# Kernel tuning notes

Measured on AMD Instinct MI355X. Metric: run time of the kernel, lower is better.

## Reference

```python
import jax, jax.numpy as jnp
import numpy as np

BN_EPS = 1e-5


def setup_inputs() -> dict:
    key = jax.random.key(0)
    ks = jax.random.split(key, 8)
    N, C, H, W = 16, 64, 56, 56
    Ch = C // 2
    x = jax.random.normal(ks[0], (N, C, H, W), dtype=jnp.float32)
    # 1x1 convs represented as [out, in] matrices
    w1 = jax.random.normal(ks[1], (Ch, C), dtype=jnp.float32) / np.sqrt(C)
    b1 = jnp.zeros((Ch,), dtype=jnp.float32)
    w2 = jax.random.normal(ks[2], (Ch, C), dtype=jnp.float32) / np.sqrt(C)
    b2 = jnp.zeros((Ch,), dtype=jnp.float32)
    w3 = jax.random.normal(ks[3], (C, C), dtype=jnp.float32) / np.sqrt(C)
    b3 = jnp.zeros((C,), dtype=jnp.float32)
    gamma = jnp.ones((C,), dtype=jnp.float32)
    beta = jnp.zeros((C,), dtype=jnp.float32)
    return {"x": x, "w1": w1, "b1": b1, "w2": w2, "b2": b2,
            "w3": w3, "b3": b3, "gamma": gamma, "beta": beta}


def _conv1x1(x, w, b):
    # x: [N,C,H,W], w: [O,C] -> [N,O,H,W]
    return jnp.einsum('nchw,oc->nohw', x, w) + b[None, :, None, None]


def reference(x, w1, b1, w2, b2, w3, b3, gamma, beta):
    N, C, H, W = x.shape
    S = H * W
    theta = _conv1x1(x, w1, b1)            # [N, C/2, H, W]
    phi = _conv1x1(x, w2, b2)              # [N, C/2, H, W]
    g = x                                  # [N, C, H, W]
    th = theta.reshape(N, -1, S)           # [N, C/2, S]
    ph = phi.reshape(N, -1, S)             # [N, C/2, S]
    gf = g.reshape(N, C, S)                # [N, C, S]
    scale = 1.0 / jnp.sqrt(jnp.float32(th.shape[1]))
    attn = jnp.einsum('nis,nit->nst', th, ph) * scale   # [N, S, S]
    attn = jax.nn.softmax(attn, axis=-1)
    f = jnp.einsum('nst,nit->nis', attn, gf).reshape(N, C, H, W)
    f = _conv1x1(f, w3, b3)
    # BatchNorm2d, training mode (batch statistics, biased variance)
    mean = jnp.mean(f, axis=(0, 2, 3), keepdims=True)
    var = jnp.mean((f - mean) ** 2, axis=(0, 2, 3), keepdims=True)
    f = (f - mean) / jnp.sqrt(var + BN_EPS)
    f = f * gamma[None, :, None, None] + beta[None, :, None, None]
    return x + f
```

## Files before the change

kernel.cpp:

```cpp
#include <hip/hip_runtime.h>
#include <hip/hip_bf16.h>

constexpr int N_ = 16, C_ = 64, CH_ = 32;
constexpr int S_ = 3136;
constexpr int SB = 64;
constexpr int NB = S_ / SB;
constexpr float SCALE = 0.17677669529663687f;
constexpr float LOG2E = 1.4426950408889634f;
constexpr float SCALE2 = SCALE * LOG2E;
constexpr float FIXM2 = 16.0f * LOG2E;

using f32x4 = __attribute__((ext_vector_type(4))) float;
using bf16x8 = __attribute__((ext_vector_type(8))) short;
using u32x2 = __attribute__((ext_vector_type(2))) unsigned;
using u32x4 = __attribute__((ext_vector_type(4))) unsigned;

__device__ __forceinline__ unsigned cvtpk(float lo, float hi) {
  unsigned r;
  asm("v_cvt_pk_bf16_f32 %0, %1, %2" : "=v"(r) : "v"(lo), "v"(hi));
  return r;
}
__device__ __forceinline__ float exp2a(float x) {
  float r;
  asm("v_exp_f32 %0, %1" : "=v"(r) : "v"(x));
  return r;
}
__device__ __forceinline__ unsigned short f2bf(float f) {
  unsigned int u = __builtin_bit_cast(unsigned int, f);
  u += 0x7fffu + ((u >> 16) & 1u);
  return (unsigned short)(u >> 16);
}

__global__ __launch_bounds__(256)
void prep_kernel(const float* __restrict__ x,
                 const float* __restrict__ w1, const float* __restrict__ b1,
                 const float* __restrict__ w2, const float* __restrict__ b2,
                 unsigned short* __restrict__ thetaT,
                 unsigned short* __restrict__ phiT,
                 unsigned short* __restrict__ xbf) {
  __shared__ float xl[64][68];
  __shared__ __align__(16) unsigned short thL[64][40];
  __shared__ __align__(16) unsigned short phL[64][40];
  const int b = blockIdx.x;
  const int n = b / NB;
  const int s0 = (b % NB) * SB;
  const int tid = threadIdx.x;
  const int sl = tid & 63;
  const int grp = tid >> 6;

#pragma unroll
  for (int cc = 0; cc < 4; ++cc) {
    int c = cc * 16 + grp * 4 + (sl >> 4);
    int s4 = (sl & 15) * 4;
    size_t gidx = (size_t)(n * C_ + c) * S_ + s0 + s4;
    f32x4 v = *(const f32x4*)(x + gidx);
    *(f32x4*)&xl[c][s4] = v;
    u32x2 pb;
    pb.x = cvtpk(v[0], v[1]);
    pb.y = cvtpk(v[2], v[3]);
    *(u32x2*)(xbf + gidx) = pb;
  }
  __syncthreads();

  float acc1[8], acc2[8];
  const int i0u = __builtin_amdgcn_readfirstlane(grp * 8);
  const float* w1b = w1 + i0u * C_;
  const float* w2b = w2 + i0u * C_;
#pragma unroll
  for (int ii = 0; ii < 8; ++ii) {
    acc1[ii] = b1[i0u + ii];
    acc2[ii] = b2[i0u + ii];
  }
#pragma unroll 1
  for (int cc = 0; cc < 4; ++cc) {
    float xv[16];
#pragma unroll
    for (int k = 0; k < 16; ++k) xv[k] = xl[cc * 16 + k][sl];
#pragma unroll
    for (int ii = 0; ii < 8; ++ii) {
#pragma unroll
      for (int k = 0; k < 16; ++k) {
        acc1[ii] = fmaf(w1b[ii * C_ + cc * 16 + k], xv[k], acc1[ii]);
        acc2[ii] = fmaf(w2b[ii * C_ + cc * 16 + k], xv[k], acc2[ii]);
      }
    }
  }
  {
    u32x4 t4, p4;
    t4.x = cvtpk(acc1[0] * SCALE2, acc1[1] * SCALE2);
    t4.y = cvtpk(acc1[2] * SCALE2, acc1[3] * SCALE2);
    t4.z = cvtpk(acc1[4] * SCALE2, acc1[5] * SCALE2);
    t4.w = cvtpk(acc1[6] * SCALE2, acc1[7] * SCALE2);
    p4.x = cvtpk(acc2[0], acc2[1]);
    p4.y = cvtpk(acc2[2], acc2[3]);
    p4.z = cvtpk(acc2[4], acc2[5]);
    p4.w = cvtpk(acc2[6], acc2[7]);
    *(u32x4*)&thL[sl][grp * 8] = t4;
    *(u32x4*)&phL[sl][grp * 8] = p4;
  }
  __syncthreads();
  {
    int row = tid >> 2, ch = (tid & 3) * 8;
    size_t o = ((size_t)(n * S_) + s0 + row) * CH_ + ch;
    *(bf16x8*)(thetaT + o) = *(const bf16x8*)&thL[row][ch];
    *(bf16x8*)(phiT + o)   = *(const bf16x8*)&phL[row][ch];
  }
}

__global__ __launch_bounds__(256)
void attn_kernel(const unsigned short* __restrict__ thetaT,
                 const unsigned short* __restrict__ phiT,
                 const unsigned short* __restrict__ xbf,
                 const float* __restrict__ w3, const float* __restrict__ b3,
                 unsigned short* __restrict__ yb, float* __restrict__ partials) {
  __shared__ __align__(16) unsigned short ldsK[2][64 * 40];
  __shared__ __align__(16) unsigned short ldsV[2][64 * 72];
  __shared__ float redS[4][128];
  const int b = (blockIdx.x & 7) * 98 + (blockIdx.x >> 3);
  const int n = b / NB;
  const int q0 = (b % NB) * SB;
  const int tid = threadIdx.x;
  const int lane = tid & 63;
  const int w = tid >> 6;
  const int l16 = lane & 15;
  const int g = lane >> 4;

  const bf16x8 qf = *(const bf16x8*)(thetaT + ((size_t)(n * S_) + q0 + w * 16 + l16) * CH_ + g * 8);

  f32x4 oacc[4];
#pragma unroll
  for (int r = 0; r < 4; ++r) oacc[r] = (f32x4){0.f, 0.f, 0.f, 0.f};
  float lsum = 0.f;
  const f32x4 cinit = (f32x4){-FIXM2, -FIXM2, -FIXM2, -FIXM2};

  const unsigned short* phiB = phiT + (size_t)n * S_ * CH_;
  const unsigned short* vB = xbf + (size_t)n * C_ * S_;

  const int krow = tid >> 2, kch = (tid & 3) * 8;
  const int vc = tid >> 3, vch = (tid & 7) * 8;

  bf16x8 kst, vst0, vst1;
  kst = *(const bf16x8*)(phiB + (size_t)krow * CH_ + kch);
  vst0 = *(const bf16x8*)(vB + (size_t)vc * S_ + vch);
  vst1 = *(const bf16x8*)(vB + (size_t)(vc + 32) * S_ + vch);
  *(bf16x8*)(ldsK[0] + krow * 40 + kch) = kst;
  *(bf16x8*)(ldsV[0] + vc * 72 + vch) = vst0;
  *(bf16x8*)(ldsV[0] + (vc + 32) * 72 + vch) = vst1;
  __syncthreads();

  int cur = 0;
#pragma unroll 1
  for (int t0 = 0; t0 < S_; t0 += 64) {
    const bool pre = (t0 + 64 < S_);
    if (pre) {
      kst = *(const bf16x8*)(phiB + (size_t)(t0 + 64 + krow) * CH_ + kch);
      vst0 = *(const bf16x8*)(vB + (size_t)vc * S_ + t0 + 64 + vch);
      vst1 = *(const bf16x8*)(vB + (size_t)(vc + 32) * S_ + t0 + 64 + vch);
    }

    const unsigned short* Kc = ldsK[cur];
    const unsigned short* Vc = ldsV[cur];
    f32x4 st[4];
    __builtin_amdgcn_s_setprio(1);
#pragma unroll
    for (int tt = 0; tt < 4; ++tt) {
      bf16x8 kf = *(const bf16x8*)(Kc + (tt * 16 + l16) * 40 + g * 8);
      st[tt] = __builtin_amdgcn_mfma_f32_16x16x32_bf16(kf, qf, cinit, 0, 0, 0);
    }
    __builtin_amdgcn_s_setprio(0);

    u32x2 pk[4];
#pragma unroll
    for (int tt = 0; tt < 4; ++tt) {
      float p0 = exp2a(st[tt][0]);
      float p1 = exp2a(st[tt][1]);
      float p2 = exp2a(st[tt][2]);
      float p3 = exp2a(st[tt][3]);
      lsum += (p0 + p1) + (p2 + p3);
      pk[tt].x = cvtpk(p0, p1);
      pk[tt].y = cvtpk(p2, p3);
    }

    __builtin_amdgcn_s_setprio(1);
#pragma unroll
    for (int h = 0; h < 2; ++h) {
      bf16x8 pf = __builtin_bit_cast(bf16x8,
          (u32x4){pk[2 * h].x, pk[2 * h].y, pk[2 * h + 1].x, pk[2 * h + 1].y});
#pragma unroll
      for (int ct = 0; ct < 4; ++ct) {
        const unsigned short* vrow = Vc + (ct * 16 + l16) * 72 + 32 * h + 4 * g;
        u32x2 v0 = *(const u32x2*)(vrow);
        u32x2 v1 = *(const u32x2*)(vrow + 16);
        bf16x8 vf = __builtin_bit_cast(bf16x8, (u32x4){v0.x, v0.y, v1.x, v1.y});
        oacc[ct] = __builtin_amdgcn_mfma_f32_16x16x32_bf16(vf, pf, oacc[ct], 0, 0, 0);
      }
    }
    __builtin_amdgcn_s_setprio(0);

    if (pre) {
      *(bf16x8*)(ldsK[cur ^ 1] + krow * 40 + kch) = kst;
      *(bf16x8*)(ldsV[cur ^ 1] + vc * 72 + vch) = vst0;
      *(bf16x8*)(ldsV[cur ^ 1] + (vc + 32) * 72 + vch) = vst1;
    }
    __syncthreads();
    cur ^= 1;
  }

  float lt = lsum;
  lt += __shfl_xor(lt, 16);
  lt += __shfl_xor(lt, 32);
  const float inv = 1.0f / lt;

  u32x4 ff[2];
#pragma unroll
  for (int m = 0; m < 2; ++m) {
    ff[m].x = cvtpk(oacc[2 * m][0] * inv, oacc[2 * m][1] * inv);
    ff[m].y = cvtpk(oacc[2 * m][2] * inv, oacc[2 * m][3] * inv);
    ff[m].z = cvtpk(oacc[2 * m + 1][0] * inv, oacc[2 * m + 1][1] * inv);
    ff[m].w = cvtpk(oacc[2 * m + 1][2] * inv, oacc[2 * m + 1][3] * inv);
  }

  const int q = q0 + w * 16 + l16;
#pragma unroll
  for (int t = 0; t < 4; ++t) {
    const float* wr = w3 + (t * 16 + l16) * C_;
    f32x4 acc = *(const f32x4*)(b3 + t * 16 + 4 * g);
#pragma unroll
    for (int m = 0; m < 2; ++m) {
      f32x4 A0 = *(const f32x4*)(wr + 32 * m + 4 * g);
      f32x4 A1 = *(const f32x4*)(wr + 32 * m + 16 + 4 * g);
      u32x4 wf;
      wf.x = cvtpk(A0[0], A0[1]);
      wf.y = cvtpk(A0[2], A0[3]);
      wf.z = cvtpk(A1[0], A1[1]);
      wf.w = cvtpk(A1[2], A1[3]);
      acc = __builtin_amdgcn_mfma_f32_16x16x32_bf16(
          __builtin_bit_cast(bf16x8, wf), __builtin_bit_cast(bf16x8, ff[m]),
          acc, 0, 0, 0);
    }
#pragma unroll
    for (int rd = 0; rd < 4; ++rd) {
      const int co = t * 16 + 4 * g + rd;
      float yv = acc[rd];
      yb[(size_t)(n * C_ + co) * S_ + q] = f2bf(yv);
      float s1 = yv, s2 = yv * yv;
#pragma unroll
      for (int off = 1; off < 16; off <<= 1) {
        s1 += __shfl_xor(s1, off);
        s2 += __shfl_xor(s2, off);
      }
      if (l16 == 0) {
        redS[w][co] = s1;
        redS[w][64 + co] = s2;
      }
    }
  }
  __syncthreads();
  if (tid < 128)
    partials[(size_t)b * 128 + tid] =
        redS[0][tid] + redS[1][tid] + redS[2][tid] + redS[3][tid];
}

__global__ __launch_bounds__(256)
void stats_kernel(const float* __restrict__ partials, float* __restrict__ stats) {
  __shared__ float red[4];
  const int c = blockIdx.x;
  const int tid = threadIdx.x;
  float s = 0.f;
  for (int r = tid; r < N_ * NB; r += 256) s += partials[(size_t)r * 128 + c];
#pragma unroll
  for (int off = 1; off < 64; off <<= 1) s += __shfl_xor(s, off);
  if ((tid & 63) == 0) red[tid >> 6] = s;
  __syncthreads();
  if (tid == 0) stats[c] = red[0] + red[1] + red[2] + red[3];
}

__global__ __launch_bounds__(256)
void bn_kernel(const float* __restrict__ x, const unsigned short* __restrict__ yb,
               const float* __restrict__ stats,
               const float* __restrict__ gamma, const float* __restrict__ beta,
               float* __restrict__ out) {
  const int idx = blockIdx.x * 256 + threadIdx.x;
  const size_t base = (size_t)idx * 8;
  const int c = (int)((base / S_) & 63);
  constexpr float invcnt = 1.0f / (N_ * S_);
  float mean = stats[c] * invcnt;
  float var = stats[64 + c] * invcnt - mean * mean;
  float a = gamma[c] * rsqrtf(var + 1e-5f);
  float bb = beta[c] - mean * a;
  u32x4 yv = *(const u32x4*)(yb + base);
#pragma unroll
  for (int h = 0; h < 2; ++h) {
    f32x4 xv = *(const f32x4*)(x + base + h * 4);
    f32x4 o;
#pragma unroll
    for (int r = 0; r < 2; ++r) {
      unsigned packed = (h * 2 + r == 0) ? yv.x : (h * 2 + r == 1) ? yv.y
                        : (h * 2 + r == 2) ? yv.z : yv.w;
      float ylo = __builtin_bit_cast(float, packed << 16);
      float yhi = __builtin_bit_cast(float, packed & 0xffff0000u);
      o[r * 2 + 0] = fmaf(ylo, a, xv[r * 2 + 0] + bb);
      o[r * 2 + 1] = fmaf(yhi, a, xv[r * 2 + 1] + bb);
    }
    *(f32x4*)(out + base + h * 4) = o;
  }
}

extern "C" void kernel_launch(void* const* d_in, const int* in_sizes, int n_in,
                              void* d_out, int out_size, void* d_ws, size_t ws_size,
                              hipStream_t stream) {
  const float* x = (const float*)d_in[0];
  const float* w1 = (const float*)d_in[1];
  const float* b1 = (const float*)d_in[2];
  const float* w2 = (const float*)d_in[3];
  const float* b2 = (const float*)d_in[4];
  const float* w3 = (const float*)d_in[5];
  const float* b3 = (const float*)d_in[6];
  const float* gamma = (const float*)d_in[7];
  const float* beta = (const float*)d_in[8];

  char* ws = (char*)d_ws;
  unsigned short* thetaT = (unsigned short*)(ws + 0);
  unsigned short* phiT   = (unsigned short*)(ws + 3211264);
  unsigned short* xbf    = (unsigned short*)(ws + 6422528);
  unsigned short* yb     = (unsigned short*)(ws + 12845056);
  float* stats           = (float*)(ws + 19267584);
  float* partials        = (float*)(ws + 19268096);
  if (ws_size < 19669504) return;

  prep_kernel<<<N_ * NB, 256, 0, stream>>>(x, w1, b1, w2, b2, thetaT, phiT, xbf);
  attn_kernel<<<N_ * NB, 256, 0, stream>>>(thetaT, phiT, xbf, w3, b3, yb, partials);
  stats_kernel<<<128, 256, 0, stream>>>(partials, stats);
  bn_kernel<<<(out_size / 8) / 256, 256, 0, stream>>>(x, yb, stats, gamma, beta, (float*)d_out);
}
```

Before: 115.0 us.

## Split key loop across two wave groups in attention kernel and merge partials

```diff
diff --git a/kernel.cpp b/kernel.cpp
--- a/kernel.cpp
+++ b/kernel.cpp
@@ -107,7 +107,7 @@
   }
 }
 
-__global__ __launch_bounds__(256)
+__global__ __launch_bounds__(512)
 void attn_kernel(const unsigned short* __restrict__ thetaT,
                  const unsigned short* __restrict__ phiT,
                  const unsigned short* __restrict__ xbf,
@@ -122,10 +122,12 @@
   const int tid = threadIdx.x;
   const int lane = tid & 63;
   const int w = tid >> 6;
+  const int qw = w & 3;
+  const int th = w >> 2;
   const int l16 = lane & 15;
   const int g = lane >> 4;
 
-  const bf16x8 qf = *(const bf16x8*)(thetaT + ((size_t)(n * S_) + q0 + w * 16 + l16) * CH_ + g * 8);
+  const bf16x8 qf = *(const bf16x8*)(thetaT + ((size_t)(n * S_) + q0 + qw * 16 + l16) * CH_ + g * 8);
 
   f32x4 oacc[4];
 #pragma unroll
@@ -136,122 +138,145 @@
   const unsigned short* phiB = phiT + (size_t)n * S_ * CH_;
   const unsigned short* vB = xbf + (size_t)n * C_ * S_;
 
-  const int krow = tid >> 2, kch = (tid & 3) * 8;
-  const int vc = tid >> 3, vch = (tid & 7) * 8;
+  const int sh = tid >> 8;
+  const int st = tid & 255;
+  const int krow = st >> 2, kch = (st & 3) * 8;
+  const int vc = st >> 3, vch = (st & 7) * 8;
 
   bf16x8 kst, vst0, vst1;
-  kst = *(const bf16x8*)(phiB + (size_t)krow * CH_ + kch);
-  vst0 = *(const bf16x8*)(vB + (size_t)vc * S_ + vch);
-  vst1 = *(const bf16x8*)(vB + (size_t)(vc + 32) * S_ + vch);
-  *(bf16x8*)(ldsK[0] + krow * 40 + kch) = kst;
-  *(bf16x8*)(ldsV[0] + vc * 72 + vch) = vst0;
-  *(bf16x8*)(ldsV[0] + (vc + 32) * 72 + vch) = vst1;
-  __syncthreads();
-
-  int cur = 0;
+  {
+    const int t0s = sh * 64;
+    kst = *(const bf16x8*)(phiB + (size_t)(t0s + krow) * CH_ + kch);
+    vst0 = *(const bf16x8*)(vB + (size_t)vc * S_ + t0s + vch);
+    vst1 = *(const bf16x8*)(vB + (size_t)(vc + 32) * S_ + t0s + vch);
+    *(bf16x8*)(ldsK[sh] + krow * 40 + kch) = kst;
+    *(bf16x8*)(ldsV[sh] + vc * 72 + vch) = vst0;
+    *(bf16x8*)(ldsV[sh] + (vc + 32) * 72 + vch) = vst1;
+  }
+  __syncthreads();
+
 #pragma unroll 1
-  for (int t0 = 0; t0 < S_; t0 += 64) {
-    const bool pre = (t0 + 64 < S_);
+  for (int pb = 0; pb < S_; pb += 128) {
+    const int tpre = pb + 128 + sh * 64;
+    const bool pre = tpre < S_;
     if (pre) {
-      kst = *(const bf16x8*)(phiB + (size_t)(t0 + 64 + krow) * CH_ + kch);
-      vst0 = *(const bf16x8*)(vB + (size_t)vc * S_ + t0 + 64 + vch);
-      vst1 = *(const bf16x8*)(vB + (size_t)(vc + 32) * S_ + t0 + 64 + vch);
-    }
-
-    const unsigned short* Kc = ldsK[cur];
-    const unsigned short* Vc = ldsV[cur];
-    f32x4 st[4];
-    __builtin_amdgcn_s_setprio(1);
-#pragma unroll
-    for (int tt = 0; tt < 4; ++tt) {
-      bf16x8 kf = *(const bf16x8*)(Kc + (tt * 16 + l16) * 40 + g * 8);
-      st[tt] = __builtin_amdgcn_mfma_f32_16x16x32_bf16(kf, qf, cinit, 0, 0, 0);
-    }
-    __builtin_amdgcn_s_setprio(0);
-
-    u32x2 pk[4];
-#pragma unroll
-    for (int tt = 0; tt < 4; ++tt) {
-      float p0 = exp2a(st[tt][0]);
-      float p1 = exp2a(st[tt][1]);
-      float p2 = exp2a(st[tt][2]);
-      float p3 = exp2a(st[tt][3]);
-      lsum += (p0 + p1) + (p2 + p3);
-      pk[tt].x = cvtpk(p0, p1);
-      pk[tt].y = cvtpk(p2, p3);
-    }
-
-    __builtin_amdgcn_s_setprio(1);
-#pragma unroll
-    for (int h = 0; h < 2; ++h) {
-      bf16x8 pf = __builtin_bit_cast(bf16x8,
-          (u32x4){pk[2 * h].x, pk[2 * h].y, pk[2 * h + 1].x, pk[2 * h + 1].y});
-#pragma unroll
-      for (int ct = 0; ct < 4; ++ct) {
-        const unsigned short* vrow = Vc + (ct * 16 + l16) * 72 + 32 * h + 4 * g;
-        u32x2 v0 = *(const u32x2*)(vrow);
-        u32x2 v1 = *(const u32x2*)(vrow + 16);
-        bf16x8 vf = __builtin_bit_cast(bf16x8, (u32x4){v0.x, v0.y, v1.x, v1.y});
-        oacc[ct] = __builtin_amdgcn_mfma_f32_16x16x32_bf16(vf, pf, oacc[ct], 0, 0, 0);
-      }
-    }
-    __builtin_amdgcn_s_setprio(0);
-
+      kst = *(const bf16x8*)(phiB + (size_t)(tpre + krow) * CH_ + kch);
+      vst0 = *(const bf16x8*)(vB + (size_t)vc * S_ + tpre + vch);
+      vst1 = *(const bf16x8*)(vB + (size_t)(vc + 32) * S_ + tpre + vch);
+    }
+
+    const int t0 = pb + th * 64;
+    if (t0 < S_) {
+      const unsigned short* Kc = ldsK[th];
+      const unsigned short* Vc = ldsV[th];
+      f32x4 st4[4];
+      __builtin_amdgcn_s_setprio(1);
+#pragma unroll
+      for (int tt = 0; tt < 4; ++tt) {
+        bf16x8 kf = *(const bf16x8*)(Kc + (tt * 16 + l16) * 40 + g * 8);
+        st4[tt] = __builtin_amdgcn_mfma_f32_16x16x32_bf16(kf, qf, cinit, 0, 0, 0);
+      }
+      __builtin_amdgcn_s_setprio(0);
+
+      u32x2 pk[4];
+#pragma unroll
+      for (int tt = 0; tt < 4; ++tt) {
+        float p0 = exp2a(st4[tt][0]);
+        float p1 = exp2a(st4[tt][1]);
+        float p2 = exp2a(st4[tt][2]);
+        float p3 = exp2a(st4[tt][3]);
+        lsum += (p0 + p1) + (p2 + p3);
+        pk[tt].x = cvtpk(p0, p1);
+        pk[tt].y = cvtpk(p2, p3);
+      }
+
+      __builtin_amdgcn_s_setprio(1);
+#pragma unroll
+      for (int h = 0; h < 2; ++h) {
+        bf16x8 pf = __builtin_bit_cast(bf16x8,
+            (u32x4){pk[2 * h].x, pk[2 * h].y, pk[2 * h + 1].x, pk[2 * h + 1].y});
+#pragma unroll
+        for (int ct = 0; ct < 4; ++ct) {
+          const unsigned short* vrow = Vc + (ct * 16 + l16) * 72 + 32 * h + 4 * g;
+          u32x2 v0 = *(const u32x2*)(vrow);
+          u32x2 v1 = *(const u32x2*)(vrow + 16);
+          bf16x8 vf = __builtin_bit_cast(bf16x8, (u32x4){v0.x, v0.y, v1.x, v1.y});
+          oacc[ct] = __builtin_amdgcn_mfma_f32_16x16x32_bf16(vf, pf, oacc[ct], 0, 0, 0);
+        }
+      }
+      __builtin_amdgcn_s_setprio(0);
+    }
+
+    __syncthreads();
     if (pre) {
-      *(bf16x8*)(ldsK[cur ^ 1] + krow * 40 + kch) = kst;
-      *(bf16x8*)(ldsV[cur ^ 1] + vc * 72 + vch) = vst0;
-      *(bf16x8*)(ldsV[cur ^ 1] + (vc + 32) * 72 + vch) = vst1;
+      *(bf16x8*)(ldsK[sh] + krow * 40 + kch) = kst;
+      *(bf16x8*)(ldsV[sh] + vc * 72 + vch) = vst0;
+      *(bf16x8*)(ldsV[sh] + (vc + 32) * 72 + vch) = vst1;
     }
     __syncthreads();
-    cur ^= 1;
-  }
-
-  float lt = lsum;
-  lt += __shfl_xor(lt, 16);
-  lt += __shfl_xor(lt, 32);
-  const float inv = 1.0f / lt;
-
-  u32x4 ff[2];
-#pragma unroll
-  for (int m = 0; m < 2; ++m) {
-    ff[m].x = cvtpk(oacc[2 * m][0] * inv, oacc[2 * m][1] * inv);
-    ff[m].y = cvtpk(oacc[2 * m][2] * inv, oacc[2 * m][3] * inv);
-    ff[m].z = cvtpk(oacc[2 * m + 1][0] * inv, oacc[2 * m + 1][1] * inv);
-    ff[m].w = cvtpk(oacc[2 * m + 1][2] * inv, oacc[2 * m + 1][3] * inv);
-  }
-
-  const int q = q0 + w * 16 + l16;
-#pragma unroll
-  for (int t = 0; t < 4; ++t) {
-    const float* wr = w3 + (t * 16 + l16) * C_;
-    f32x4 acc = *(const f32x4*)(b3 + t * 16 + 4 * g);
+  }
+
+  float* mrg = (float*)&ldsV[0][0];
+  if (th == 1) {
+    float* p = mrg + ((size_t)(qw * 64 + lane)) * 18;
+#pragma unroll
+    for (int ct = 0; ct < 4; ++ct) *(f32x4*)(p + ct * 4) = oacc[ct];
+    p[16] = lsum;
+  }
+  __syncthreads();
+  if (th == 0) {
+    float* p = mrg + ((size_t)(qw * 64 + lane)) * 18;
+#pragma unroll
+    for (int ct = 0; ct < 4; ++ct) oacc[ct] += *(const f32x4*)(p + ct * 4);
+    lsum += p[16];
+
+    float lt = lsum;
+    lt += __shfl_xor(lt, 16);
+    lt += __shfl_xor(lt, 32);
+    const float inv = 1.0f / lt;
+
+    u32x4 ff[2];
 #pragma unroll
     for (int m = 0; m < 2; ++m) {
-      f32x4 A0 = *(const f32x4*)(wr + 32 * m + 4 * g);
-      f32x4 A1 = *(const f32x4*)(wr + 32 * m + 16 + 4 * g);
-      u32x4 wf;
-      wf.x = cvtpk(A0[0], A0[1]);
-      wf.y = cvtpk(A0[2], A0[3]);
-      wf.z = cvtpk(A1[0], A1[1]);
-      wf.w = cvtpk(A1[2], A1[3]);
-      acc = __builtin_amdgcn_mfma_f32_16x16x32_bf16(
-          __builtin_bit_cast(bf16x8, wf), __builtin_bit_cast(bf16x8, ff[m]),
-          acc, 0, 0, 0);
-    }
-#pragma unroll
-    for (int rd = 0; rd < 4; ++rd) {
-      const int co = t * 16 + 4 * g + rd;
-      float yv = acc[rd];
-      yb[(size_t)(n * C_ + co) * S_ + q] = f2bf(yv);
-      float s1 = yv, s2 = yv * yv;
-#pragma unroll
-      for (int off = 1; off < 16; off <<= 1) {
-        s1 += __shfl_xor(s1, off);
-        s2 += __shfl_xor(s2, off);
-      }
-      if (l16 == 0) {
-        redS[w][co] = s1;
-        redS[w][64 + co] = s2;
+      ff[m].x = cvtpk(oacc[2 * m][0] * inv, oacc[2 * m][1] * inv);
+      ff[m].y = cvtpk(oacc[2 * m][2] * inv, oacc[2 * m][3] * inv);
+      ff[m].z = cvtpk(oacc[2 * m + 1][0] * inv, oacc[2 * m + 1][1] * inv);
+      ff[m].w = cvtpk(oacc[2 * m + 1][2] * inv, oacc[2 * m + 1][3] * inv);
+    }
+
+    const int q = q0 + qw * 16 + l16;
+#pragma unroll
+    for (int t = 0; t < 4; ++t) {
+      const float* wr = w3 + (t * 16 + l16) * C_;
+      f32x4 acc = *(const f32x4*)(b3 + t * 16 + 4 * g);
+#pragma unroll
+      for (int m = 0; m < 2; ++m) {
+        f32x4 A0 = *(const f32x4*)(wr + 32 * m + 4 * g);
+        f32x4 A1 = *(const f32x4*)(wr + 32 * m + 16 + 4 * g);
+        u32x4 wf;
+        wf.x = cvtpk(A0[0], A0[1]);
+        wf.y = cvtpk(A0[2], A0[3]);
+        wf.z = cvtpk(A1[0], A1[1]);
+        wf.w = cvtpk(A1[2], A1[3]);
+        acc = __builtin_amdgcn_mfma_f32_16x16x32_bf16(
+            __builtin_bit_cast(bf16x8, wf), __builtin_bit_cast(bf16x8, ff[m]),
+            acc, 0, 0, 0);
+      }
+#pragma unroll
+      for (int rd = 0; rd < 4; ++rd) {
+        const int co = t * 16 + 4 * g + rd;
+        float yv = acc[rd];
+        yb[(size_t)(n * C_ + co) * S_ + q] = f2bf(yv);
+        float s1 = yv, s2 = yv * yv;
+#pragma unroll
+        for (int off = 1; off < 16; off <<= 1) {
+          s1 += __shfl_xor(s1, off);
+          s2 += __shfl_xor(s2, off);
+        }
+        if (l16 == 0) {
+          redS[qw][co] = s1;
+          redS[qw][64 + co] = s2;
+        }
       }
     }
   }
@@ -329,7 +354,7 @@
   if (ws_size < 19669504) return;
 
   prep_kernel<<<N_ * NB, 256, 0, stream>>>(x, w1, b1, w2, b2, thetaT, phiT, xbf);
-  attn_kernel<<<N_ * NB, 256, 0, stream>>>(thetaT, phiT, xbf, w3, b3, yb, partials);
+  attn_kernel<<<N_ * NB, 512, 0, stream>>>(thetaT, phiT, xbf, w3, b3, yb, partials);
   stats_kernel<<<128, 256, 0, stream>>>(partials, stats);
   bn_kernel<<<(out_size / 8) / 256, 256, 0, stream>>>(x, yb, stats, gamma, beta, (float*)d_out);
 }
```

Result: slower. 125.3 us (+8.9%).

## Switch attention to 32x32x16 MFMA with key-split waves and LDS merge

Applied to the files above, without the earlier changes.

```diff
diff --git a/kernel.cpp b/kernel.cpp
--- a/kernel.cpp
+++ b/kernel.cpp
@@ -11,6 +11,7 @@
 constexpr float FIXM2 = 16.0f * LOG2E;
 
 using f32x4 = __attribute__((ext_vector_type(4))) float;
+using f32x16 = __attribute__((ext_vector_type(16))) float;
 using bf16x8 = __attribute__((ext_vector_type(8))) short;
 using u32x2 = __attribute__((ext_vector_type(2))) unsigned;
 using u32x4 = __attribute__((ext_vector_type(4))) unsigned;
@@ -115,23 +116,32 @@
                  unsigned short* __restrict__ yb, float* __restrict__ partials) {
   __shared__ __align__(16) unsigned short ldsK[2][64 * 40];
   __shared__ __align__(16) unsigned short ldsV[2][64 * 72];
-  __shared__ float redS[4][128];
+  __shared__ float redS[2][128];
   const int b = (blockIdx.x & 7) * 98 + (blockIdx.x >> 3);
   const int n = b / NB;
   const int q0 = (b % NB) * SB;
   const int tid = threadIdx.x;
   const int lane = tid & 63;
   const int w = tid >> 6;
-  const int l16 = lane & 15;
-  const int g = lane >> 4;
-
-  const bf16x8 qf = *(const bf16x8*)(thetaT + ((size_t)(n * S_) + q0 + w * 16 + l16) * CH_ + g * 8);
-
-  f32x4 oacc[4];
-#pragma unroll
-  for (int r = 0; r < 4; ++r) oacc[r] = (f32x4){0.f, 0.f, 0.f, 0.f};
+  const int qw = w & 1;
+  const int th = w >> 1;
+  const int cl = lane & 31;
+  const int h = lane >> 5;
+
+  const unsigned short* thQ =
+      thetaT + ((size_t)(n * S_) + q0 + qw * 32 + cl) * CH_;
+  const bf16x8 qfA = *(const bf16x8*)(thQ + h * 8);
+  const bf16x8 qfB = *(const bf16x8*)(thQ + 16 + h * 8);
+
+  f32x16 oacc[2];
+#pragma unroll
+  for (int cb = 0; cb < 2; ++cb)
+#pragma unroll
+    for (int r = 0; r < 16; ++r) oacc[cb][r] = 0.f;
   float lsum = 0.f;
-  const f32x4 cinit = (f32x4){-FIXM2, -FIXM2, -FIXM2, -FIXM2};
+  f32x16 cinit;
+#pragma unroll
+  for (int r = 0; r < 16; ++r) cinit[r] = -FIXM2;
 
   const unsigned short* phiB = phiT + (size_t)n * S_ * CH_;
   const unsigned short* vB = xbf + (size_t)n * C_ * S_;
@@ -160,39 +170,38 @@
 
     const unsigned short* Kc = ldsK[cur];
     const unsigned short* Vc = ldsV[cur];
-    f32x4 st[4];
+
+    const unsigned short* kr = Kc + (th * 32 + cl) * 40 + h * 8;
+    bf16x8 kfA = *(const bf16x8*)(kr);
+    bf16x8 kfB = *(const bf16x8*)(kr + 16);
     __builtin_amdgcn_s_setprio(1);
-#pragma unroll
-    for (int tt = 0; tt < 4; ++tt) {
-      bf16x8 kf = *(const bf16x8*)(Kc + (tt * 16 + l16) * 40 + g * 8);
-      st[tt] = __builtin_amdgcn_mfma_f32_16x16x32_bf16(kf, qf, cinit, 0, 0, 0);
-    }
+    f32x16 st = __builtin_amdgcn_mfma_f32_32x32x16_bf16(kfA, qfA, cinit, 0, 0, 0);
+    st = __builtin_amdgcn_mfma_f32_32x32x16_bf16(kfB, qfB, st, 0, 0, 0);
     __builtin_amdgcn_s_setprio(0);
 
-    u32x2 pk[4];
-#pragma unroll
-    for (int tt = 0; tt < 4; ++tt) {
-      float p0 = exp2a(st[tt][0]);
-      float p1 = exp2a(st[tt][1]);
-      float p2 = exp2a(st[tt][2]);
-      float p3 = exp2a(st[tt][3]);
-      lsum += (p0 + p1) + (p2 + p3);
-      pk[tt].x = cvtpk(p0, p1);
-      pk[tt].y = cvtpk(p2, p3);
-    }
+    float p[16];
+#pragma unroll
+    for (int r = 0; r < 16; ++r) {
+      p[r] = exp2a(st[r]);
+      lsum += p[r];
+    }
+    unsigned pkw[8];
+#pragma unroll
+    for (int i = 0; i < 8; ++i) pkw[i] = cvtpk(p[2 * i], p[2 * i + 1]);
 
     __builtin_amdgcn_s_setprio(1);
 #pragma unroll
-    for (int h = 0; h < 2; ++h) {
+    for (int tb = 0; tb < 2; ++tb) {
       bf16x8 pf = __builtin_bit_cast(bf16x8,
-          (u32x4){pk[2 * h].x, pk[2 * h].y, pk[2 * h + 1].x, pk[2 * h + 1].y});
-#pragma unroll
-      for (int ct = 0; ct < 4; ++ct) {
-        const unsigned short* vrow = Vc + (ct * 16 + l16) * 72 + 32 * h + 4 * g;
-        u32x2 v0 = *(const u32x2*)(vrow);
-        u32x2 v1 = *(const u32x2*)(vrow + 16);
+          (u32x4){pkw[tb * 4 + 0], pkw[tb * 4 + 1], pkw[tb * 4 + 2], pkw[tb * 4 + 3]});
+#pragma unroll
+      for (int cb = 0; cb < 2; ++cb) {
+        const unsigned short* vr =
+            Vc + (cb * 32 + cl) * 72 + th * 32 + tb * 16 + 4 * h;
+        u32x2 v0 = *(const u32x2*)(vr);
+        u32x2 v1 = *(const u32x2*)(vr + 8);
         bf16x8 vf = __builtin_bit_cast(bf16x8, (u32x4){v0.x, v0.y, v1.x, v1.y});
-        oacc[ct] = __builtin_amdgcn_mfma_f32_16x16x32_bf16(vf, pf, oacc[ct], 0, 0, 0);
+        oacc[cb] = __builtin_amdgcn_mfma_f32_32x32x16_bf16(vf, pf, oacc[cb], 0, 0, 0);
       }
     }
     __builtin_amdgcn_s_setprio(0);
@@ -206,59 +215,101 @@
     cur ^= 1;
   }
 
-  float lt = lsum;
-  lt += __shfl_xor(lt, 16);
-  lt += __shfl_xor(lt, 32);
-  const float inv = 1.0f / lt;
-
-  u32x4 ff[2];
-#pragma unroll
-  for (int m = 0; m < 2; ++m) {
-    ff[m].x = cvtpk(oacc[2 * m][0] * inv, oacc[2 * m][1] * inv);
-    ff[m].y = cvtpk(oacc[2 * m][2] * inv, oacc[2 * m][3] * inv);
-    ff[m].z = cvtpk(oacc[2 * m + 1][0] * inv, oacc[2 * m + 1][1] * inv);
-    ff[m].w = cvtpk(oacc[2 * m + 1][2] * inv, oacc[2 * m + 1][3] * inv);
-  }
-
-  const int q = q0 + w * 16 + l16;
-#pragma unroll
-  for (int t = 0; t < 4; ++t) {
-    const float* wr = w3 + (t * 16 + l16) * C_;
-    f32x4 acc = *(const f32x4*)(b3 + t * 16 + 4 * g);
-#pragma unroll
-    for (int m = 0; m < 2; ++m) {
-      f32x4 A0 = *(const f32x4*)(wr + 32 * m + 4 * g);
-      f32x4 A1 = *(const f32x4*)(wr + 32 * m + 16 + 4 * g);
-      u32x4 wf;
-      wf.x = cvtpk(A0[0], A0[1]);
-      wf.y = cvtpk(A0[2], A0[3]);
-      wf.z = cvtpk(A1[0], A1[1]);
-      wf.w = cvtpk(A1[2], A1[3]);
-      acc = __builtin_amdgcn_mfma_f32_16x16x32_bf16(
-          __builtin_bit_cast(bf16x8, wf), __builtin_bit_cast(bf16x8, ff[m]),
-          acc, 0, 0, 0);
-    }
-#pragma unroll
-    for (int rd = 0; rd < 4; ++rd) {
-      const int co = t * 16 + 4 * g + rd;
-      float yv = acc[rd];
-      yb[(size_t)(n * C_ + co) * S_ + q] = f2bf(yv);
-      float s1 = yv, s2 = yv * yv;
-#pragma unroll
-      for (int off = 1; off < 16; off <<= 1) {
-        s1 += __shfl_xor(s1, off);
-        s2 += __shfl_xor(s2, off);
-      }
-      if (l16 == 0) {
-        redS[w][co] = s1;
-        redS[w][64 + co] = s2;
+  float* mrg = (float*)&ldsV[0][0];
+  if (th == 1) {
+    float* pm = mrg + ((size_t)(qw * 64 + lane)) * 36;
+#pragma unroll
+    for (int cb = 0; cb < 2; ++cb)
+#pragma unroll
+      for (int i = 0; i < 4; ++i) {
+        f32x4 v = {oacc[cb][4 * i], oacc[cb][4 * i + 1],
+                   oacc[cb][4 * i + 2], oacc[cb][4 * i + 3]};
+        *(f32x4*)(pm + cb * 16 + 4 * i) = v;
+      }
+    pm[32] = lsum;
+  }
+  __syncthreads();
+  if (th == 0) {
+    float* pm = mrg + ((size_t)(qw * 64 + lane)) * 36;
+#pragma unroll
+    for (int cb = 0; cb < 2; ++cb)
+#pragma unroll
+      for (int i = 0; i < 4; ++i) {
+        f32x4 v = *(const f32x4*)(pm + cb * 16 + 4 * i);
+        oacc[cb][4 * i] += v[0];
+        oacc[cb][4 * i + 1] += v[1];
+        oacc[cb][4 * i + 2] += v[2];
+        oacc[cb][4 * i + 3] += v[3];
+      }
+    lsum += pm[32];
+
+    float lt = lsum;
+    lt += __shfl_xor(lt, 32);
+    const float inv = 1.0f / lt;
+
+    unsigned ff[4][4];
+#pragma unroll
+    for (int kb = 0; kb < 4; ++kb) {
+      const int blk = kb >> 1, rb = (kb & 1) * 8;
+#pragma unroll
+      for (int i = 0; i < 4; ++i)
+        ff[kb][i] = cvtpk(oacc[blk][rb + 2 * i] * inv,
+                          oacc[blk][rb + 2 * i + 1] * inv);
+    }
+
+    const int q = q0 + qw * 32 + cl;
+#pragma unroll
+    for (int ch32 = 0; ch32 < 2; ++ch32) {
+      const float* wr = w3 + (ch32 * 32 + cl) * C_;
+      f32x16 acc;
+      {
+        f32x4 b0 = *(const f32x4*)(b3 + ch32 * 32 + 4 * h);
+        f32x4 b1v = *(const f32x4*)(b3 + ch32 * 32 + 8 + 4 * h);
+        f32x4 b2v = *(const f32x4*)(b3 + ch32 * 32 + 16 + 4 * h);
+        f32x4 b3v = *(const f32x4*)(b3 + ch32 * 32 + 24 + 4 * h);
+#pragma unroll
+        for (int i = 0; i < 4; ++i) {
+          acc[i] = b0[i];
+          acc[4 + i] = b1v[i];
+          acc[8 + i] = b2v[i];
+          acc[12 + i] = b3v[i];
+        }
+      }
+#pragma unroll
+      for (int kb = 0; kb < 4; ++kb) {
+        f32x4 a0 = *(const f32x4*)(wr + kb * 16 + 4 * h);
+        f32x4 a1 = *(const f32x4*)(wr + kb * 16 + 8 + 4 * h);
+        u32x4 wf;
+        wf.x = cvtpk(a0[0], a0[1]);
+        wf.y = cvtpk(a0[2], a0[3]);
+        wf.z = cvtpk(a1[0], a1[1]);
+        wf.w = cvtpk(a1[2], a1[3]);
+        bf16x8 fb = __builtin_bit_cast(bf16x8,
+            (u32x4){ff[kb][0], ff[kb][1], ff[kb][2], ff[kb][3]});
+        acc = __builtin_amdgcn_mfma_f32_32x32x16_bf16(
+            __builtin_bit_cast(bf16x8, wf), fb, acc, 0, 0, 0);
+      }
+#pragma unroll
+      for (int r = 0; r < 16; ++r) {
+        const int co = ch32 * 32 + (r & 3) + 8 * (r >> 2) + 4 * h;
+        float yv = acc[r];
+        yb[(size_t)(n * C_ + co) * S_ + q] = f2bf(yv);
+        float s1 = yv, s2 = yv * yv;
+#pragma unroll
+        for (int off = 1; off < 32; off <<= 1) {
+          s1 += __shfl_xor(s1, off);
+          s2 += __shfl_xor(s2, off);
+        }
+        if (cl == 0) {
+          redS[qw][co] = s1;
+          redS[qw][64 + co] = s2;
+        }
       }
     }
   }
   __syncthreads();
   if (tid < 128)
-    partials[(size_t)b * 128 + tid] =
-        redS[0][tid] + redS[1][tid] + redS[2][tid] + redS[3][tid];
+    partials[(size_t)b * 128 + tid] = redS[0][tid] + redS[1][tid];
 }
 
 __global__ __launch_bounds__(256)
@@ -290,19 +341,19 @@
   float bb = beta[c] - mean * a;
   u32x4 yv = *(const u32x4*)(yb + base);
 #pragma unroll
-  for (int h = 0; h < 2; ++h) {
-    f32x4 xv = *(const f32x4*)(x + base + h * 4);
+  for (int hh = 0; hh < 2; ++hh) {
+    f32x4 xv = *(const f32x4*)(x + base + hh * 4);
     f32x4 o;
 #pragma unroll
     for (int r = 0; r < 2; ++r) {
-      unsigned packed = (h * 2 + r == 0) ? yv.x : (h * 2 + r == 1) ? yv.y
-                        : (h * 2 + r == 2) ? yv.z : yv.w;
+      unsigned packed = (hh * 2 + r == 0) ? yv.x : (hh * 2 + r == 1) ? yv.y
+                        : (hh * 2 + r == 2) ? yv.z : yv.w;
       float ylo = __builtin_bit_cast(float, packed << 16);
       float yhi = __builtin_bit_cast(float, packed & 0xffff0000u);
       o[r * 2 + 0] = fmaf(ylo, a, xv[r * 2 + 0] + bb);
       o[r * 2 + 1] = fmaf(yhi, a, xv[r * 2 + 1] + bb);
     }
-    *(f32x4*)(out + base + h * 4) = o;
+    *(f32x4*)(out + base + hh * 4) = o;
   }
 }
 
```

After: 102.6 us (median of 2 runs). 10.8% less time.
